# Kernel tuning notes

Hardware: AMD Instinct MI355X
Metric: run time of the kernel (lower is better)

The kernel has to match this reference:

```python
import jax, jax.numpy as jnp
import numpy as np

D = 512      # embeddings_dim (in_features == out_features)
H = 4        # num_heads
MID = 2048   # mid_features
B, S = 4, 2048
EPS = 1e-5


def _ln(x, g, b):
    mu = jnp.mean(x, axis=-1, keepdims=True)
    var = jnp.mean(jnp.square(x - mu), axis=-1, keepdims=True)
    return g * (x - mu) / jnp.sqrt(var + EPS) + b


def setup_inputs() -> dict:
    key = jax.random.key(0)
    ks = jax.random.split(key, 16)
    w = 0.02  # weight init scale
    return {
        "x_encoder": jax.random.normal(ks[0], (B, S, D), jnp.float32),
        "x_decoder": jax.random.normal(ks[1], (B, S, D), jnp.float32),
        # per-head full-width projections (each head is a D->D Linear)
        "Wq": jax.random.normal(ks[2], (H, D, D), jnp.float32) * w,
        "bq": jnp.zeros((H, D), jnp.float32),
        "Wk": jax.random.normal(ks[3], (H, D, D), jnp.float32) * w,
        "bk": jnp.zeros((H, D), jnp.float32),
        "Wv": jax.random.normal(ks[4], (H, D, D), jnp.float32) * w,
        "bv": jnp.zeros((H, D), jnp.float32),
        # out_reshaper: Rearrange('b h s d -> b s (d h)') then Linear(D*H -> D)
        "Wo": jax.random.normal(ks[5], (D * H, D), jnp.float32) * w,
        "bo": jnp.zeros((D,), jnp.float32),
        "ln1_g": jnp.ones((D,), jnp.float32), "ln1_b": jnp.zeros((D,), jnp.float32),
        "ln2_g": jnp.ones((D,), jnp.float32), "ln2_b": jnp.zeros((D,), jnp.float32),
        # FouriFeedForward: D -> MID -> D with SELU
        "W1": jax.random.normal(ks[6], (D, MID), jnp.float32) * w,
        "b1": jnp.zeros((MID,), jnp.float32),
        "W2": jax.random.normal(ks[7], (MID, D), jnp.float32) * w,
        "b2": jnp.zeros((D,), jnp.float32),
        "ln3_g": jnp.ones((D,), jnp.float32), "ln3_b": jnp.zeros((D,), jnp.float32),
    }


def reference(x_encoder, x_decoder, Wq, bq, Wk, bk, Wv, bv, Wo, bo,
              ln1_g, ln1_b, ln2_g, ln2_b, W1, b1, W2, b2, ln3_g, ln3_b):
    # Fourier token mixing: per-batch fftn over (seq, feature) dims, keep real part
    xf = jnp.fft.fftn(x_decoder, axes=(1, 2)).real
    xd = _ln(x_decoder + xf, ln1_g, ln1_b)  # [B,S,D]

    # Linear multi-head attention: q from decoder, k/v from encoder.
    # qs/ks/vs: [B,H,S,D]; softmax over the HEAD axis (dim=1 in torch)
    qs = jax.nn.softmax(jnp.einsum('bsd,hde->bhse', xd, Wq) + bq[None, :, None, :], axis=1)
    ks = jax.nn.softmax(jnp.einsum('bsd,hde->bhse', x_encoder, Wk) + bk[None, :, None, :], axis=1)
    vs = jnp.einsum('bsd,hde->bhse', x_encoder, Wv) + bv[None, :, None, :]

    gc = jnp.einsum('bhsd,bhse->bhde', ks, vs)       # [B,H,D,D] global contexts
    out = jnp.einsum('bhsd,bhde->bhse', qs, gc)      # [B,H,S,D]

    # Rearrange 'b h s d -> b s (d h)': d is the slow axis, h the fast axis
    b, h, s, d = out.shape
    out = out.transpose(0, 2, 3, 1).reshape(b, s, d * h)
    attn = out @ Wo + bo                              # [B,S,D]

    x = _ln(xd + attn, ln2_g, ln2_b)
    ff = jax.nn.selu(x @ W1 + b1) @ W2 + b2           # dropout_p=0 (eval)
    x = _ln(x + ff, ln3_g, ln3_b)
    return x
```

## Files before the change

kernel.cpp:

```cpp
#include <hip/hip_runtime.h>
#include <stdint.h>

typedef __bf16 bf16;
typedef __bf16 bf16x8 __attribute__((ext_vector_type(8)));
typedef float f32x4 __attribute__((ext_vector_type(4)));

static __device__ __forceinline__ void async16(const void* g, void* l) {
  __builtin_amdgcn_global_load_lds(
      (__attribute__((address_space(1))) void*)g,
      (__attribute__((address_space(3))) void*)l, 16, 0, 0);
}

__global__ void __launch_bounds__(256) prep_all(
    const float* __restrict__ xdec, const float* __restrict__ xenc,
    bf16* __restrict__ Ttrig, bf16* __restrict__ Atrig2,
    bf16* __restrict__ xdec_b, bf16* __restrict__ xenc_b,
    const float* __restrict__ Wq, const float* __restrict__ Wk,
    const float* __restrict__ Wv, const float* __restrict__ Wo,
    const float* __restrict__ W1, const float* __restrict__ W2,
    bf16* __restrict__ BtQ, bf16* __restrict__ BtK, bf16* __restrict__ BtV,
    bf16* __restrict__ WoTh, bf16* __restrict__ W1T, bf16* __restrict__ W2T) {
  __shared__ bf16 tile[32][33];
  int id = blockIdx.x;
  if (id < 2048) {
    int idx = id * 256 + threadIdx.x;
    int d = idx & 511, jp = idx >> 9;
    int jj = jp >> 1, p = jp & 1;
    int t = (d * jj) & 511;
    float ang = (float)t * (6.283185307179586f / 512.0f);
    Ttrig[idx] = (bf16)(p ? __sinf(ang) : __cosf(ang));
  } else if (id < 11840) {
    int idx = (id - 2048) * 256 + threadIdx.x;
    int k = idx % 1088;
    int rr = idx / 1088;
    int r = rr % 1152, half = rr / 1152;
    float v = 0.0f;
    int tt = (r * k) & 2047;
    float ang = (float)tt * (6.283185307179586f / 2048.0f);
    if (half == 0) { if (r <= 1024 && k <= 1024) v = __cosf(ang); }
    else           { if (r <= 1023 && k >= 1 && k <= 1023) v = -__sinf(ang); }
    Atrig2[idx] = (bf16)v;
  } else if (id < 15936) {
    int i = ((id - 11840) * 256 + threadIdx.x) * 4;
    float4 v = *(const float4*)(xdec + i);
    bf16 o[4] __attribute__((aligned(8))) =
        {(bf16)v.x, (bf16)v.y, (bf16)v.z, (bf16)v.w};
    *(uint2*)(xdec_b + i) = *(const uint2*)o;
  } else if (id < 20032) {
    int i = ((id - 15936) * 256 + threadIdx.x) * 4;
    float4 v = *(const float4*)(xenc + i);
    bf16 o[4] __attribute__((aligned(8))) =
        {(bf16)v.x, (bf16)v.y, (bf16)v.z, (bf16)v.w};
    *(uint2*)(xenc_b + i) = *(const uint2*)o;
  } else {
    int id2 = id - 20032;
    int kind = id2 >> 10, t = id2 & 1023;
    const float* in; bf16* out; int R, C, rt, ct;
    bool iperm = false, hsel = false; int hh = 0;
    if (kind == 0)      { in = Wq; out = BtQ; R = 2048; C = 512; rt = t >> 4; ct = t & 15; iperm = true; }
    else if (kind == 1) { in = Wk; out = BtK; R = 2048; C = 512; rt = t >> 4; ct = t & 15; iperm = true; }
    else if (kind == 2) { in = Wv; out = BtV; R = 2048; C = 512; rt = t >> 4; ct = t & 15; iperm = true; }
    else if (kind == 3) {
      int zz = t >> 8, tt = t & 255;
      in = Wo; out = WoTh + (long)zz * 262144;
      R = 512; C = 512; rt = tt >> 4; ct = tt & 15; hsel = true; hh = zz;
    }
    else if (kind == 4) { in = W1; out = W1T; R = 512; C = 2048; rt = t >> 6; ct = t & 63; }
    else                { in = W2; out = W2T; R = 2048; C = 512; rt = t >> 4; ct = t & 15; }
    int c0 = ct * 32, r0 = rt * 32;
    int tx = threadIdx.x & 31, ty = threadIdx.x >> 5;
#pragma unroll
    for (int i = 0; i < 32; i += 8) {
      int r = r0 + ty + i;
      int rr = hsel ? (4 * r + hh) : r;
      tile[ty + i][tx] = (bf16)in[(long)rr * C + (c0 + tx)];
    }
    __syncthreads();
#pragma unroll
    for (int i = 0; i < 32; i += 8) {
      int cc = c0 + ty + i, rr = r0 + tx;
      if (iperm) {
        int e = cc, h = rr >> 9;
        int n = (e & 15) | (h << 4) | ((e >> 4) << 6);
        out[((long)n << 9) + (rr & 511)] = tile[tx][ty + i];
      } else {
        out[(long)cc * R + rr] = tile[tx][ty + i];
      }
    }
  }
}

__global__ void __launch_bounds__(256) fold_y(const bf16* __restrict__ Yt,
                                              bf16* __restrict__ Yf2) {
  int idx2 = blockIdx.x * 256 + threadIdx.x;
  int k2 = (idx2 % 544) * 2;
  int rr = idx2 / 544;
  int j = rr & 511, z = rr >> 9;
  int b = z & 3, half = z >> 2;
  const bf16* yin = Yt + (long)b * 2097152 + (long)j * 4096;
  bf16 o[2] __attribute__((aligned(4)));
  if (half == 0) {
    bf16 f[2] __attribute__((aligned(4)));
    *(uint*)f = *(const uint*)(yin + k2);
    float r0 = (float)yin[2048 - k2];
    float r1 = (float)yin[2047 - k2];
    float v0, v1;
    if (k2 == 0)            v0 = (float)f[0];
    else if (k2 == 1024)    v0 = (float)f[0];
    else if (k2 < 1024)     v0 = (float)f[0] + r0;
    else                    v0 = 0.0f;
    if (k2 + 1 < 1024)      v1 = (float)f[1] + r1;
    else                    v1 = 0.0f;
    o[0] = (bf16)v0; o[1] = (bf16)v1;
  } else {
    bf16 f[2] __attribute__((aligned(4)));
    *(uint*)f = *(const uint*)(yin + 2048 + k2);
    float r0 = (float)yin[4096 - k2];
    float r1 = (float)yin[4095 - k2];
    float v0, v1;
    if (k2 >= 1 && k2 <= 1023) v0 = (float)f[0] - r0; else v0 = 0.0f;
    if (k2 + 1 <= 1023)        v1 = (float)f[1] - r1; else v1 = 0.0f;
    o[0] = (bf16)v0; o[1] = (bf16)v1;
  }
  *(uint*)(Yf2 + (long)z * 557056 + (long)j * 1088 + k2) = *(const uint*)o;
}

__global__ void __launch_bounds__(256) ln1_kernel(
    const float* __restrict__ xdec, const bf16* __restrict__ CSb,
    const float* __restrict__ g, const float* __restrict__ be,
    bf16* __restrict__ outb) {
  const int row = blockIdx.x, t = threadIdx.x;
  const int b = row >> 11, s = row & 2047;
  const int sp = (s <= 1024) ? s : 2048 - s;
  const float sgn = (s <= 1024) ? 1.0f : -1.0f;
  const bf16* Crow = CSb + ((long)b * 1152 + sp) * 512;
  const bf16* Srow = CSb + ((long)(b + 4) * 1152 + sp) * 512;
  const long base = (long)row * 512;
  float2 xp = *(const float2*)(xdec + base + 2 * t);
  bf16 cp[2] __attribute__((aligned(4)));
  bf16 spv[2] __attribute__((aligned(4)));
  *(uint*)cp = *(const uint*)(Crow + 2 * t);
  *(uint*)spv = *(const uint*)(Srow + 2 * t);
  float v0 = xp.x + (float)cp[0] + sgn * (float)spv[0];
  float v1 = xp.y + (float)cp[1] + sgn * (float)spv[1];
  float sm = v0 + v1, q = v0 * v0 + v1 * v1;
#pragma unroll
  for (int off = 32; off > 0; off >>= 1) {
    sm += __shfl_down(sm, off);
    q += __shfl_down(q, off);
  }
  __shared__ float red[8];
  const int wv = t >> 6, ln = t & 63;
  if (ln == 0) { red[wv] = sm; red[wv + 4] = q; }
  __syncthreads();
  float S = red[0] + red[1] + red[2] + red[3];
  float Q = red[4] + red[5] + red[6] + red[7];
  float mu = S * (1.0f / 512.0f);
  float var = Q * (1.0f / 512.0f) - mu * mu;
  float rstd = rsqrtf(var + 1e-5f);
  float2 gp = *(const float2*)(g + 2 * t);
  float2 bp = *(const float2*)(be + 2 * t);
  bf16 op[2] __attribute__((aligned(4)));
  op[0] = (bf16)(gp.x * (v0 - mu) * rstd + bp.x);
  op[1] = (bf16)(gp.y * (v1 - mu) * rstd + bp.y);
  *(uint*)(outb + base + 2 * t) = *(const uint*)op;
}

template <int WRITE_BF16, int WRITE_F32>
__global__ void __launch_bounds__(256) ln_kernel(
    const bf16* __restrict__ A, const bf16* __restrict__ Bv,
    const float* __restrict__ g, const float* __restrict__ be,
    bf16* __restrict__ outb, float* __restrict__ outf) {
  const int row = blockIdx.x, t = threadIdx.x;
  const long base = (long)row * 512;
  bf16 ap[2] __attribute__((aligned(4)));
  bf16 bpv[2] __attribute__((aligned(4)));
  *(uint*)ap = *(const uint*)(A + base + 2 * t);
  *(uint*)bpv = *(const uint*)(Bv + base + 2 * t);
  float v0 = (float)ap[0] + (float)bpv[0];
  float v1 = (float)ap[1] + (float)bpv[1];
  float s = v0 + v1, q = v0 * v0 + v1 * v1;
#pragma unroll
  for (int off = 32; off > 0; off >>= 1) {
    s += __shfl_down(s, off);
    q += __shfl_down(q, off);
  }
  __shared__ float red[8];
  const int wv = t >> 6, ln = t & 63;
  if (ln == 0) { red[wv] = s; red[wv + 4] = q; }
  __syncthreads();
  float S = red[0] + red[1] + red[2] + red[3];
  float Q = red[4] + red[5] + red[6] + red[7];
  float mu = S * (1.0f / 512.0f);
  float var = Q * (1.0f / 512.0f) - mu * mu;
  float rstd = rsqrtf(var + 1e-5f);
  float2 gp = *(const float2*)(g + 2 * t);
  float2 bp = *(const float2*)(be + 2 * t);
  float o0 = gp.x * (v0 - mu) * rstd + bp.x;
  float o1 = gp.y * (v1 - mu) * rstd + bp.y;
  if (WRITE_BF16) {
    bf16 op[2] __attribute__((aligned(4)));
    op[0] = (bf16)o0; op[1] = (bf16)o1;
    *(uint*)(outb + base + 2 * t) = *(const uint*)op;
  }
  if (WRITE_F32) {
    float2 of; of.x = o0; of.y = o1;
    *(float2*)(outf + base + 2 * t) = of;
  }
}

template <int BN, int ADDR_MODE, int HAS_BIAS, int DO_SELU, int F32OUT, int SWIZ,
          int AHEAD>
static __device__ __forceinline__ void gemm_bt_body(
    int id, bf16* lA, bf16* lB,
    const bf16* __restrict__ A, const bf16* __restrict__ Bt,
    const float* __restrict__ bias, void* __restrict__ Cout,
    int N, int K, long sAz, long sBz, long sBiasz, long sCz,
    int gx, int gy, int gin) {
  int x, y, z;
  {
    if (SWIZ == 0) {
      x = id % gx; int t2 = id / gx; y = t2 % gy; z = t2 / gy;
    } else {
      int xcd = id & 7, r = id >> 3;
      int inner = r % gin, G = xcd + 8 * (r / gin);
      if (SWIZ == 1)      { y = G; x = inner % gx; z = inner / gx; }
      else if (SWIZ == 2) { z = G; x = inner % gx; y = inner / gx; }
      else                { x = G; y = inner % gy; z = inner / gy; }
    }
  }
  A  += (AHEAD == 1) ? sAz * (z & 3) : (AHEAD == 2) ? sAz * (z >> 2) : sAz * z;
  Bt += sBz * z;
  const int m0 = y * 128, n0 = x * BN;
  const int t = threadIdx.x;
  const int lane = t & 63, wave = t >> 6;
  const int srow = t >> 3;
  const int pch  = t & 7;
  const int lch  = pch ^ (srow & 7);
  const bf16* Ag = A  + (long)(m0 + srow) * K + lch * 8;
  const bf16* Bg = Bt + (long)(n0 + srow) * K + lch * 8;
  bf16* lAp = lA + srow * 64 + pch * 8;
  bf16* lBp = lB + srow * 64 + pch * 8;
  constexpr int MI = (BN == 128) ? 4 : 2;
  const int wm = (BN == 128) ? (wave >> 1) * 64 : wave * 32;
  const int wn = (BN == 128) ? (wave & 1) * 64 : 0;
  const int fr = lane & 15, fq = lane >> 4;

  f32x4 acc[MI][4] = {};

  for (int k0 = 0; k0 < K; k0 += 64) {
    __syncthreads();
#pragma unroll
    for (int i = 0; i < 4; ++i)
      async16(Ag + k0 + (long)(32 * i) * K, lAp + 32 * i * 64);
#pragma unroll
    for (int i = 0; i < BN / 32; ++i)
      async16(Bg + k0 + (long)(32 * i) * K, lBp + 32 * i * 64);
    __syncthreads();
#pragma unroll
    for (int kk = 0; kk < 2; ++kk) {
      bf16x8 av[MI], bfrag[4];
#pragma unroll
      for (int mi = 0; mi < MI; ++mi) {
        int r = wm + mi * 16 + fr;
        int c = (kk * 4 + fq) ^ (r & 7);
        av[mi] = *(const bf16x8*)&lA[r * 64 + c * 8];
      }
#pragma unroll
      for (int ni = 0; ni < 4; ++ni) {
        int r = wn + ni * 16 + fr;
        int c = (kk * 4 + fq) ^ (r & 7);
        bfrag[ni] = *(const bf16x8*)&lB[r * 64 + c * 8];
      }
#pragma unroll
      for (int mi = 0; mi < MI; ++mi)
#pragma unroll
        for (int ni = 0; ni < 4; ++ni)
          acc[mi][ni] = __builtin_amdgcn_mfma_f32_16x16x32_bf16(
              av[mi], bfrag[ni], acc[mi][ni], 0, 0, 0);
    }
  }

#pragma unroll
  for (int mi = 0; mi < MI; ++mi) {
#pragma unroll
    for (int ni = 0; ni < 4; ++ni) {
      const int col = n0 + wn + ni * 16 + fr;
      float bias_v = 0.0f;
      if (HAS_BIAS == 1) bias_v = bias[sBiasz * z + col];
      if (ADDR_MODE == 9) {
        const int b = z >> 2, h = z & 3;
        const int kidx = (col & 15) | (h << 4) | ((col >> 4) << 6);
#pragma unroll
        for (int r = 0; r < 4; ++r) {
          const int row = m0 + wm + mi * 16 + fq * 4 + r;
          ((bf16*)Cout)[((long)(b * 512 + row)) * 2048 + kidx] =
              (bf16)(acc[mi][ni][r] + bias_v);
        }
      } else {
#pragma unroll
        for (int r = 0; r < 4; ++r) {
          const int row = m0 + wm + mi * 16 + fq * 4 + r;
          float v = acc[mi][ni][r] + bias_v;
          if (DO_SELU) v = v > 0.0f ? 1.0507009873554805f * v
                                    : 1.7580993408473766f * (__expf(v) - 1.0f);
          long addr = sCz * z + (long)row * N + col;
          if (F32OUT) ((float*)Cout)[addr] = v;
          else        ((bf16*)Cout)[addr] = (bf16)v;
        }
      }
    }
  }
}

template <int BN, int ADDR_MODE, int HAS_BIAS, int DO_SELU, int F32OUT, int SWIZ,
          int AHEAD = 0>
__global__ void __launch_bounds__(256, 2) gemm_bt(
    const bf16* __restrict__ A, const bf16* __restrict__ Bt,
    const float* __restrict__ bias, void* __restrict__ Cout,
    int N, int K, long sAz, long sBz, long sBiasz, long sCz,
    int gx, int gy, int gin) {
  __shared__ __align__(16) bf16 lA[128 * 64];
  __shared__ __align__(16) bf16 lB[BN * 64];
  gemm_bt_body<BN, ADDR_MODE, HAS_BIAS, DO_SELU, F32OUT, SWIZ, AHEAD>(
      blockIdx.x, lA, lB, A, Bt, bias, Cout, N, K, sAz, sBz, sBiasz, sCz, gx, gy, gin);
}

static __device__ __forceinline__ void qkv_body(
    int id, bf16* lA, bf16* lB,
    const bf16* __restrict__ Aq, const bf16* __restrict__ Aenc,
    const bf16* __restrict__ BQ, const bf16* __restrict__ BK,
    const bf16* __restrict__ BV,
    const float* __restrict__ bq, const float* __restrict__ bk,
    const float* __restrict__ bv,
    bf16* __restrict__ qs2, bf16* __restrict__ ksT, bf16* __restrict__ vsT) {
  const int seg = id >> 10, sid = id & 1023;
  const int xcd = sid & 7, r = sid >> 3;
  const int x = r & 15, y = xcd + 8 * (r >> 4);
  const bf16 *A, *Bt; bf16* out; const float* bias;
  if (seg == 0)      { A = Aq;   Bt = BQ; out = qs2; bias = bq; }
  else if (seg == 1) { A = Aenc; Bt = BK; out = ksT; bias = bk; }
  else               { A = Aenc; Bt = BV; out = vsT; bias = bv; }
  const int K = 512;
  const int m0 = y * 128, n0 = x * 128;
  const int t = threadIdx.x;
  const int lane = t & 63, wave = t >> 6;
  const int srow = t >> 3, pch = t & 7, lch = pch ^ (srow & 7);
  const bf16* Ag = A  + (long)(m0 + srow) * K + lch * 8;
  const bf16* Bg = Bt + (long)(n0 + srow) * K + lch * 8;
  bf16* lAp = lA + srow * 64 + pch * 8;
  bf16* lBp = lB + srow * 64 + pch * 8;
  const int wm = (wave >> 1) * 64, wn = (wave & 1) * 64;
  const int fr = lane & 15, fq = lane >> 4;

  f32x4 acc[4][4] = {};
  for (int k0 = 0; k0 < K; k0 += 64) {
    __syncthreads();
#pragma unroll
    for (int i = 0; i < 4; ++i) {
      async16(Ag + k0 + (long)(32 * i) * K, lAp + 32 * i * 64);
      async16(Bg + k0 + (long)(32 * i) * K, lBp + 32 * i * 64);
    }
    __syncthreads();
#pragma unroll
    for (int kk = 0; kk < 2; ++kk) {
      bf16x8 av[4], bfrag[4];
#pragma unroll
      for (int mi = 0; mi < 4; ++mi) {
        int rr = wm + mi * 16 + fr;
        int c = (kk * 4 + fq) ^ (rr & 7);
        av[mi] = *(const bf16x8*)&lA[rr * 64 + c * 8];
      }
#pragma unroll
      for (int ni = 0; ni < 4; ++ni) {
        int rr = wn + ni * 16 + fr;
        int c = (kk * 4 + fq) ^ (rr & 7);
        bfrag[ni] = *(const bf16x8*)&lB[rr * 64 + c * 8];
      }
#pragma unroll
      for (int mi = 0; mi < 4; ++mi)
#pragma unroll
        for (int ni = 0; ni < 4; ++ni)
          acc[mi][ni] = __builtin_amdgcn_mfma_f32_16x16x32_bf16(
              av[mi], bfrag[ni], acc[mi][ni], 0, 0, 0);
    }
  }

  const int ebase = fr + 16 * ((n0 + wn) >> 6);
  const float b0 = bias[ebase], b1 = bias[512 + ebase],
              b2 = bias[1024 + ebase], b3 = bias[1536 + ebase];
  if (seg == 0) {
#pragma unroll
    for (int mi = 0; mi < 4; ++mi) {
#pragma unroll
      for (int r = 0; r < 4; ++r) {
        const int row = m0 + wm + mi * 16 + fq * 4 + r;
        float v0 = acc[mi][0][r] + b0;
        float v1 = acc[mi][1][r] + b1;
        float v2 = acc[mi][2][r] + b2;
        float v3 = acc[mi][3][r] + b3;
        float m = fmaxf(fmaxf(v0, v1), fmaxf(v2, v3));
        float p0 = __expf(v0 - m), p1 = __expf(v1 - m),
              p2 = __expf(v2 - m), p3 = __expf(v3 - m);
        float rs = 1.0f / (p0 + p1 + p2 + p3);
        const long ob = (long)row * 2048 + n0 + wn + fr;
        out[ob]      = (bf16)(p0 * rs);
        out[ob + 16] = (bf16)(p1 * rs);
        out[ob + 32] = (bf16)(p2 * rs);
        out[ob + 48] = (bf16)(p3 * rs);
      }
    }
  } else {
    bf16* lT = lA;
    const int bb = m0 >> 11;
    const int s_tile = m0 & 2047;
    const int e_loc = fr + 16 * (wn >> 6);
    __syncthreads();
#pragma unroll
    for (int mi = 0; mi < 4; ++mi) {
      const int s0 = wm + mi * 16 + fq * 4;
      bf16 tmp[4][4] __attribute__((aligned(8)));
#pragma unroll
      for (int r = 0; r < 4; ++r) {
        float v0 = acc[mi][0][r] + b0;
        float v1 = acc[mi][1][r] + b1;
        float v2 = acc[mi][2][r] + b2;
        float v3 = acc[mi][3][r] + b3;
        if (seg == 1) {
          float m = fmaxf(fmaxf(v0, v1), fmaxf(v2, v3));
          float p0 = __expf(v0 - m), p1 = __expf(v1 - m),
                p2 = __expf(v2 - m), p3 = __expf(v3 - m);
          float rs = 1.0f / (p0 + p1 + p2 + p3);
          v0 = p0 * rs; v1 = p1 * rs; v2 = p2 * rs; v3 = p3 * rs;
        }
        tmp[0][r] = (bf16)v0; tmp[1][r] = (bf16)v1;
        tmp[2][r] = (bf16)v2; tmp[3][r] = (bf16)v3;
      }
#pragma unroll
      for (int ni = 0; ni < 4; ++ni) {
        const int row = ni * 32 + e_loc;
        const int el = row * 128 + ((((s0 >> 3) ^ (row & 15)) << 3) | (s0 & 7));
        *(uint2*)&lT[el] = *(const uint2*)tmp[ni];
      }
    }
    __syncthreads();
    const int c = lane & 15, rg = lane >> 4;
#pragma unroll
    for (int i = 0; i < 8; ++i) {
      const int row = wave * 32 + rg + i * 4;
      const int el = row * 128 + ((c ^ (row & 15)) << 3);
      uint4 v = *(const uint4*)&lT[el];
      const int h = row >> 5, e = (row & 31) + 32 * x;
      *(uint4*)(out + ((long)((bb * 4 + h) * 512 + e)) * 2048 + s_tile + c * 8) = v;
    }
  }
}

__global__ void __launch_bounds__(256, 2) fused_kv_yt(
    const bf16* __restrict__ Aenc, const bf16* __restrict__ BK,
    const bf16* __restrict__ BV,
    const float* __restrict__ bk, const float* __restrict__ bv,
    bf16* __restrict__ ksT, bf16* __restrict__ vsT,
    const bf16* __restrict__ Ttrig, const bf16* __restrict__ xdec_b,
    bf16* __restrict__ Yt) {
  __shared__ __align__(16) bf16 smem[16384];
  int id = blockIdx.x;
  if (id < 2048)
    qkv_body(id + 1024, smem, smem + 8192, nullptr, Aenc, nullptr, BK, BV,
             nullptr, bk, bv, nullptr, ksT, vsT);
  else
    gemm_bt_body<128, 0, 0, 0, 0, 3, 0>(id - 2048, smem, smem + 8192,
        Ttrig, xdec_b, nullptr, Yt, 2048, 512, 0L, 1048576L, 0L, 2097152L, 16, 8, 32);
}

__global__ void __launch_bounds__(256, 2) fused_gc_cs(
    const bf16* __restrict__ ksT, const bf16* __restrict__ vsT,
    bf16* __restrict__ gc,
    const bf16* __restrict__ Atrig2, const bf16* __restrict__ Yf2,
    bf16* __restrict__ CSb) {
  __shared__ __align__(16) bf16 smem[12288];
  int id = blockIdx.x;
  if (id < 512)
    gemm_bt_body<64, 0, 0, 0, 0, 2, 0>(id, smem, smem + 8192,
        ksT, vsT, nullptr, gc, 512, 2048, 1048576L, 1048576L, 0L, 262144L, 8, 4, 32);
  else
    gemm_bt_body<64, 0, 0, 0, 0, 2, 2>(id - 512, smem, smem + 8192,
        Atrig2, Yf2, nullptr, CSb, 512, 1088, 1253376L, 557056L, 0L, 589824L, 8, 9, 72);
}

__global__ void __launch_bounds__(256, 2) fused_q_gw(
    const bf16* __restrict__ Aq, const bf16* __restrict__ BQ,
    const float* __restrict__ bq, bf16* __restrict__ qs2,
    const bf16* __restrict__ WoTh, const bf16* __restrict__ gc,
    bf16* __restrict__ gwT) {
  __shared__ __align__(16) bf16 smem[16384];
  int id = blockIdx.x;
  if (id < 1024)
    qkv_body(id, smem, smem + 8192, Aq, nullptr, BQ, nullptr, nullptr,
             bq, nullptr, nullptr, qs2, nullptr, nullptr);
  else
    gemm_bt_body<64, 9, 0, 0, 0, 2, 1>(id - 1024, smem, smem + 8192,
        WoTh, gc, nullptr, gwT, 512, 512, 262144L, 262144L, 0L, 0L, 8, 4, 32);
}

extern "C" void kernel_launch(void* const* d_in, const int* in_sizes, int n_in,
                              void* d_out, int out_size, void* d_ws, size_t ws_size,
                              hipStream_t stream) {
  (void)in_sizes; (void)n_in; (void)out_size; (void)ws_size;
  const float* x_enc = (const float*)d_in[0];
  const float* x_dec = (const float*)d_in[1];
  const float* Wq = (const float*)d_in[2];
  const float* bq = (const float*)d_in[3];
  const float* Wk = (const float*)d_in[4];
  const float* bk = (const float*)d_in[5];
  const float* Wv = (const float*)d_in[6];
  const float* bv = (const float*)d_in[7];
  const float* Wo = (const float*)d_in[8];
  const float* bo = (const float*)d_in[9];
  const float* g1 = (const float*)d_in[10];
  const float* be1 = (const float*)d_in[11];
  const float* g2 = (const float*)d_in[12];
  const float* be2 = (const float*)d_in[13];
  const float* W1 = (const float*)d_in[14];
  const float* b1 = (const float*)d_in[15];
  const float* W2 = (const float*)d_in[16];
  const float* b2 = (const float*)d_in[17];
  const float* g3 = (const float*)d_in[18];
  const float* be3 = (const float*)d_in[19];

  char* ws = (char*)d_ws;
  const size_t MB = 1u << 20;
  bf16*  BtQ    = (bf16*) (ws + 0);
  bf16*  midb   = (bf16*) (ws + 0);
  bf16*  ksT    = (bf16*) (ws + 32 * MB);
  bf16*  attn_b = (bf16*) (ws + 32 * MB);
  bf16*  vsT    = (bf16*) (ws + 64 * MB);
  bf16*  ff_b   = (bf16*) (ws + 72 * MB);
  bf16*  Atrig2 = (bf16*) (ws + 96 * MB);
  bf16*  Ttrig  = (bf16*) (ws + 101 * MB);
  bf16*  CSb    = (bf16*) (ws + 102 * MB);
  bf16*  qs2    = (bf16*) (ws + 96 * MB);
  bf16*  xenc_b = (bf16*) (ws + 128 * MB);
  bf16*  BtK    = (bf16*) (ws + 136 * MB);
  bf16*  BtV    = (bf16*) (ws + 138 * MB);
  bf16*  xd_b   = (bf16*) (ws + 192 * MB);
  bf16*  x2_b   = (bf16*) (ws + 200 * MB);
  bf16*  gwT    = (bf16*) (ws + 208 * MB);
  bf16*  Yt     = (bf16*) (ws + 216 * MB);
  bf16*  gc     = (bf16*) (ws + 216 * MB);
  bf16*  Yf2    = (bf16*) (ws + 232 * MB);
  bf16*  WoTh   = (bf16*) (ws + 241 * MB);
  bf16*  W1T    = (bf16*) (ws + 243 * MB);
  bf16*  W2T    = (bf16*) (ws + 245 * MB);
  bf16*  xdec_b = (bf16*) (ws + 247 * MB);

  prep_all<<<26176, 256, 0, stream>>>(x_dec, x_enc, Ttrig, Atrig2, xdec_b, xenc_b,
                                      Wq, Wk, Wv, Wo, W1, W2,
                                      BtQ, BtK, BtV, WoTh, W1T, W2T);

  fused_kv_yt<<<2560, 256, 0, stream>>>(xenc_b, BtK, BtV, bk, bv, ksT, vsT,
                                        Ttrig, xdec_b, Yt);

  fold_y<<<8704, 256, 0, stream>>>(Yt, Yf2);

  fused_gc_cs<<<1088, 256, 0, stream>>>(ksT, vsT, gc, Atrig2, Yf2, CSb);

  ln1_kernel<<<8192, 256, 0, stream>>>(x_dec, CSb, g1, be1, xd_b);

  fused_q_gw<<<1536, 256, 0, stream>>>(xd_b, BtQ, bq, qs2, WoTh, gc, gwT);

  gemm_bt<64, 0, 1, 0, 0, 1><<<512, 256, 0, stream>>>(
      qs2, gwT, bo, attn_b, 512, 2048, 4194304L, 1048576L, 0L, 1048576L, 8, 16, 32);
  ln_kernel<1, 0><<<8192, 256, 0, stream>>>(
      xd_b, attn_b, g2, be2, x2_b, nullptr);

  gemm_bt<128, 0, 1, 1, 0, 1><<<1024, 256, 0, stream>>>(
      x2_b, W1T, b1, midb, 2048, 512, 0L, 0L, 0L, 0L, 16, 64, 16);
  gemm_bt<64, 0, 1, 0, 0, 1><<<512, 256, 0, stream>>>(
      midb, W2T, b2, ff_b, 512, 2048, 0L, 0L, 0L, 0L, 8, 64, 8);
  ln_kernel<0, 1><<<8192, 256, 0, stream>>>(
      x2_b, ff_b, g3, be3, nullptr, (float*)d_out);
}
```

Measured before the change: 366.6 us.

## Fuse K and V projections sharing encoder tile; vectorize trig and fold kernels

New measurement: 355.6 us. 3.0% less time.

```diff
diff --git a/kernel.cpp b/kernel.cpp
--- a/kernel.cpp
+++ b/kernel.cpp
@@ -22,38 +22,49 @@
     bf16* __restrict__ WoTh, bf16* __restrict__ W1T, bf16* __restrict__ W2T) {
   __shared__ bf16 tile[32][33];
   int id = blockIdx.x;
-  if (id < 2048) {
+  if (id < 512) {
     int idx = id * 256 + threadIdx.x;
-    int d = idx & 511, jp = idx >> 9;
+    int d0 = (idx & 127) * 4, jp = idx >> 7;
     int jj = jp >> 1, p = jp & 1;
-    int t = (d * jj) & 511;
-    float ang = (float)t * (6.283185307179586f / 512.0f);
-    Ttrig[idx] = (bf16)(p ? __sinf(ang) : __cosf(ang));
-  } else if (id < 11840) {
-    int idx = (id - 2048) * 256 + threadIdx.x;
-    int k = idx % 1088;
-    int rr = idx / 1088;
+    bf16 o[4] __attribute__((aligned(8)));
+#pragma unroll
+    for (int i = 0; i < 4; ++i) {
+      int tt = ((d0 + i) * jj) & 511;
+      float ang = (float)tt * (6.283185307179586f / 512.0f);
+      o[i] = (bf16)(p ? __sinf(ang) : __cosf(ang));
+    }
+    *(uint2*)(Ttrig + jp * 512 + d0) = *(const uint2*)o;
+  } else if (id < 2960) {
+    int idx = (id - 512) * 256 + threadIdx.x;
+    int k0 = (idx % 272) * 4;
+    int rr = idx / 272;
     int r = rr % 1152, half = rr / 1152;
-    float v = 0.0f;
-    int tt = (r * k) & 2047;
-    float ang = (float)tt * (6.283185307179586f / 2048.0f);
-    if (half == 0) { if (r <= 1024 && k <= 1024) v = __cosf(ang); }
-    else           { if (r <= 1023 && k >= 1 && k <= 1023) v = -__sinf(ang); }
-    Atrig2[idx] = (bf16)v;
-  } else if (id < 15936) {
-    int i = ((id - 11840) * 256 + threadIdx.x) * 4;
+    bf16 o[4] __attribute__((aligned(8)));
+#pragma unroll
+    for (int i = 0; i < 4; ++i) {
+      int k = k0 + i;
+      float v = 0.0f;
+      int tt = (r * k) & 2047;
+      float ang = (float)tt * (6.283185307179586f / 2048.0f);
+      if (half == 0) { if (r <= 1024 && k <= 1024) v = __cosf(ang); }
+      else           { if (r <= 1023 && k >= 1 && k <= 1023) v = -__sinf(ang); }
+      o[i] = (bf16)v;
+    }
+    *(uint2*)(Atrig2 + (long)rr * 1088 + k0) = *(const uint2*)o;
+  } else if (id < 7056) {
+    int i = ((id - 2960) * 256 + threadIdx.x) * 4;
     float4 v = *(const float4*)(xdec + i);
     bf16 o[4] __attribute__((aligned(8))) =
         {(bf16)v.x, (bf16)v.y, (bf16)v.z, (bf16)v.w};
     *(uint2*)(xdec_b + i) = *(const uint2*)o;
-  } else if (id < 20032) {
-    int i = ((id - 15936) * 256 + threadIdx.x) * 4;
+  } else if (id < 11152) {
+    int i = ((id - 7056) * 256 + threadIdx.x) * 4;
     float4 v = *(const float4*)(xenc + i);
     bf16 o[4] __attribute__((aligned(8))) =
         {(bf16)v.x, (bf16)v.y, (bf16)v.z, (bf16)v.w};
     *(uint2*)(xenc_b + i) = *(const uint2*)o;
   } else {
-    int id2 = id - 20032;
+    int id2 = id - 11152;
     int kind = id2 >> 10, t = id2 & 1023;
     const float* in; bf16* out; int R, C, rt, ct;
     bool iperm = false, hsel = false; int hh = 0;
@@ -92,37 +103,38 @@
 
 __global__ void __launch_bounds__(256) fold_y(const bf16* __restrict__ Yt,
                                               bf16* __restrict__ Yf2) {
-  int idx2 = blockIdx.x * 256 + threadIdx.x;
-  int k2 = (idx2 % 544) * 2;
-  int rr = idx2 / 544;
+  int idx = blockIdx.x * 256 + threadIdx.x;
+  int k0 = (idx % 272) * 4;
+  int rr = idx / 272;
   int j = rr & 511, z = rr >> 9;
   int b = z & 3, half = z >> 2;
   const bf16* yin = Yt + (long)b * 2097152 + (long)j * 4096;
-  bf16 o[2] __attribute__((aligned(4)));
+  bf16 o[4] __attribute__((aligned(8)));
   if (half == 0) {
-    bf16 f[2] __attribute__((aligned(4)));
-    *(uint*)f = *(const uint*)(yin + k2);
-    float r0 = (float)yin[2048 - k2];
-    float r1 = (float)yin[2047 - k2];
-    float v0, v1;
-    if (k2 == 0)            v0 = (float)f[0];
-    else if (k2 == 1024)    v0 = (float)f[0];
-    else if (k2 < 1024)     v0 = (float)f[0] + r0;
-    else                    v0 = 0.0f;
-    if (k2 + 1 < 1024)      v1 = (float)f[1] + r1;
-    else                    v1 = 0.0f;
-    o[0] = (bf16)v0; o[1] = (bf16)v1;
+    bf16 f[4] __attribute__((aligned(8)));
+    *(uint2*)f = *(const uint2*)(yin + k0);
+#pragma unroll
+    for (int i = 0; i < 4; ++i) {
+      int k = k0 + i;
+      float v;
+      if (k == 0)            v = (float)f[0];
+      else if (k == 1024)    v = (float)f[i];
+      else if (k < 1024)     v = (float)f[i] + (float)yin[2048 - k];
+      else                   v = 0.0f;
+      o[i] = (bf16)v;
+    }
   } else {
-    bf16 f[2] __attribute__((aligned(4)));
-    *(uint*)f = *(const uint*)(yin + 2048 + k2);
-    float r0 = (float)yin[4096 - k2];
-    float r1 = (float)yin[4095 - k2];
-    float v0, v1;
-    if (k2 >= 1 && k2 <= 1023) v0 = (float)f[0] - r0; else v0 = 0.0f;
-    if (k2 + 1 <= 1023)        v1 = (float)f[1] - r1; else v1 = 0.0f;
-    o[0] = (bf16)v0; o[1] = (bf16)v1;
-  }
-  *(uint*)(Yf2 + (long)z * 557056 + (long)j * 1088 + k2) = *(const uint*)o;
+    bf16 f[4] __attribute__((aligned(8)));
+    *(uint2*)f = *(const uint2*)(yin + 2048 + k0);
+#pragma unroll
+    for (int i = 0; i < 4; ++i) {
+      int k = k0 + i;
+      float v = 0.0f;
+      if (k >= 1 && k <= 1023) v = (float)f[i] - (float)yin[4096 - k];
+      o[i] = (bf16)v;
+    }
+  }
+  *(uint2*)(Yf2 + (long)z * 557056 + (long)j * 1088 + k0) = *(const uint2*)o;
 }
 
 __global__ void __launch_bounds__(256) ln1_kernel(
@@ -334,13 +346,11 @@
     const float* __restrict__ bq, const float* __restrict__ bk,
     const float* __restrict__ bv,
     bf16* __restrict__ qs2, bf16* __restrict__ ksT, bf16* __restrict__ vsT) {
-  const int seg = id >> 10, sid = id & 1023;
+  const int sid = id & 1023;
   const int xcd = sid & 7, r = sid >> 3;
   const int x = r & 15, y = xcd + 8 * (r >> 4);
-  const bf16 *A, *Bt; bf16* out; const float* bias;
-  if (seg == 0)      { A = Aq;   Bt = BQ; out = qs2; bias = bq; }
-  else if (seg == 1) { A = Aenc; Bt = BK; out = ksT; bias = bk; }
-  else               { A = Aenc; Bt = BV; out = vsT; bias = bv; }
+  const bf16 *A = Aq, *Bt = BQ; bf16* out = qs2; const float* bias = bq;
+  (void)Aenc; (void)BK; (void)BV; (void)bk; (void)bv; (void)ksT; (void)vsT;
   const int K = 512;
   const int m0 = y * 128, n0 = x * 128;
   const int t = threadIdx.x;
@@ -389,70 +399,164 @@
   const int ebase = fr + 16 * ((n0 + wn) >> 6);
   const float b0 = bias[ebase], b1 = bias[512 + ebase],
               b2 = bias[1024 + ebase], b3 = bias[1536 + ebase];
-  if (seg == 0) {
-#pragma unroll
-    for (int mi = 0; mi < 4; ++mi) {
-#pragma unroll
-      for (int r = 0; r < 4; ++r) {
-        const int row = m0 + wm + mi * 16 + fq * 4 + r;
-        float v0 = acc[mi][0][r] + b0;
-        float v1 = acc[mi][1][r] + b1;
-        float v2 = acc[mi][2][r] + b2;
-        float v3 = acc[mi][3][r] + b3;
-        float m = fmaxf(fmaxf(v0, v1), fmaxf(v2, v3));
-        float p0 = __expf(v0 - m), p1 = __expf(v1 - m),
-              p2 = __expf(v2 - m), p3 = __expf(v3 - m);
-        float rs = 1.0f / (p0 + p1 + p2 + p3);
-        const long ob = (long)row * 2048 + n0 + wn + fr;
-        out[ob]      = (bf16)(p0 * rs);
-        out[ob + 16] = (bf16)(p1 * rs);
-        out[ob + 32] = (bf16)(p2 * rs);
-        out[ob + 48] = (bf16)(p3 * rs);
-      }
-    }
-  } else {
-    bf16* lT = lA;
-    const int bb = m0 >> 11;
-    const int s_tile = m0 & 2047;
-    const int e_loc = fr + 16 * (wn >> 6);
+#pragma unroll
+  for (int mi = 0; mi < 4; ++mi) {
+#pragma unroll
+    for (int r = 0; r < 4; ++r) {
+      const int row = m0 + wm + mi * 16 + fq * 4 + r;
+      float v0 = acc[mi][0][r] + b0;
+      float v1 = acc[mi][1][r] + b1;
+      float v2 = acc[mi][2][r] + b2;
+      float v3 = acc[mi][3][r] + b3;
+      float m = fmaxf(fmaxf(v0, v1), fmaxf(v2, v3));
+      float p0 = __expf(v0 - m), p1 = __expf(v1 - m),
+            p2 = __expf(v2 - m), p3 = __expf(v3 - m);
+      float rs = 1.0f / (p0 + p1 + p2 + p3);
+      const long ob = (long)row * 2048 + n0 + wn + fr;
+      out[ob]      = (bf16)(p0 * rs);
+      out[ob + 16] = (bf16)(p1 * rs);
+      out[ob + 32] = (bf16)(p2 * rs);
+      out[ob + 48] = (bf16)(p3 * rs);
+    }
+  }
+}
+
+static __device__ __forceinline__ void kv2_body(
+    int sid, bf16* smem,
+    const bf16* __restrict__ Aenc, const bf16* __restrict__ BK,
+    const bf16* __restrict__ BV,
+    const float* __restrict__ bk, const float* __restrict__ bv,
+    bf16* __restrict__ ksT, bf16* __restrict__ vsT) {
+  const int xcd = sid & 7, r = sid >> 3;
+  const int x = r & 15, y = xcd + 8 * (r >> 4);
+  const int K = 512;
+  const int m0 = y * 128, n0 = x * 128;
+  const int t = threadIdx.x;
+  const int lane = t & 63, wave = t >> 6;
+  const int srow = t >> 3, pch = t & 7, lch = pch ^ (srow & 7);
+  bf16* lA  = smem;
+  bf16* lBK = smem + 8192;
+  bf16* lBV = smem + 16384;
+  const bf16* Ag  = Aenc + (long)(m0 + srow) * K + lch * 8;
+  const bf16* BKg = BK   + (long)(n0 + srow) * K + lch * 8;
+  const bf16* BVg = BV   + (long)(n0 + srow) * K + lch * 8;
+  bf16* lAp  = lA  + srow * 64 + pch * 8;
+  bf16* lBKp = lBK + srow * 64 + pch * 8;
+  bf16* lBVp = lBV + srow * 64 + pch * 8;
+  const int wm = (wave >> 1) * 64, wn = (wave & 1) * 64;
+  const int fr = lane & 15, fq = lane >> 4;
+
+  f32x4 accK[4][4] = {}, accV[4][4] = {};
+  for (int k0 = 0; k0 < K; k0 += 64) {
     __syncthreads();
 #pragma unroll
-    for (int mi = 0; mi < 4; ++mi) {
-      const int s0 = wm + mi * 16 + fq * 4;
-      bf16 tmp[4][4] __attribute__((aligned(8)));
-#pragma unroll
-      for (int r = 0; r < 4; ++r) {
-        float v0 = acc[mi][0][r] + b0;
-        float v1 = acc[mi][1][r] + b1;
-        float v2 = acc[mi][2][r] + b2;
-        float v3 = acc[mi][3][r] + b3;
-        if (seg == 1) {
-          float m = fmaxf(fmaxf(v0, v1), fmaxf(v2, v3));
-          float p0 = __expf(v0 - m), p1 = __expf(v1 - m),
-                p2 = __expf(v2 - m), p3 = __expf(v3 - m);
-          float rs = 1.0f / (p0 + p1 + p2 + p3);
-          v0 = p0 * rs; v1 = p1 * rs; v2 = p2 * rs; v3 = p3 * rs;
+    for (int i = 0; i < 4; ++i) {
+      async16(Ag  + k0 + (long)(32 * i) * K, lAp  + 32 * i * 64);
+      async16(BKg + k0 + (long)(32 * i) * K, lBKp + 32 * i * 64);
+      async16(BVg + k0 + (long)(32 * i) * K, lBVp + 32 * i * 64);
+    }
+    __syncthreads();
+#pragma unroll
+    for (int kk = 0; kk < 2; ++kk) {
+      bf16x8 av[4], bkf[4], bvf[4];
+#pragma unroll
+      for (int mi = 0; mi < 4; ++mi) {
+        int rr = wm + mi * 16 + fr;
+        int c = (kk * 4 + fq) ^ (rr & 7);
+        av[mi] = *(const bf16x8*)&lA[rr * 64 + c * 8];
+      }
+#pragma unroll
+      for (int ni = 0; ni < 4; ++ni) {
+        int rr = wn + ni * 16 + fr;
+        int c = (kk * 4 + fq) ^ (rr & 7);
+        bkf[ni] = *(const bf16x8*)&lBK[rr * 64 + c * 8];
+        bvf[ni] = *(const bf16x8*)&lBV[rr * 64 + c * 8];
+      }
+#pragma unroll
+      for (int mi = 0; mi < 4; ++mi)
+#pragma unroll
+        for (int ni = 0; ni < 4; ++ni) {
+          accK[mi][ni] = __builtin_amdgcn_mfma_f32_16x16x32_bf16(
+              av[mi], bkf[ni], accK[mi][ni], 0, 0, 0);
+          accV[mi][ni] = __builtin_amdgcn_mfma_f32_16x16x32_bf16(
+              av[mi], bvf[ni], accV[mi][ni], 0, 0, 0);
         }
-        tmp[0][r] = (bf16)v0; tmp[1][r] = (bf16)v1;
-        tmp[2][r] = (bf16)v2; tmp[3][r] = (bf16)v3;
-      }
-#pragma unroll
-      for (int ni = 0; ni < 4; ++ni) {
-        const int row = ni * 32 + e_loc;
-        const int el = row * 128 + ((((s0 >> 3) ^ (row & 15)) << 3) | (s0 & 7));
-        *(uint2*)&lT[el] = *(const uint2*)tmp[ni];
-      }
-    }
-    __syncthreads();
-    const int c = lane & 15, rg = lane >> 4;
-#pragma unroll
-    for (int i = 0; i < 8; ++i) {
-      const int row = wave * 32 + rg + i * 4;
-      const int el = row * 128 + ((c ^ (row & 15)) << 3);
-      uint4 v = *(const uint4*)&lT[el];
-      const int h = row >> 5, e = (row & 31) + 32 * x;
-      *(uint4*)(out + ((long)((bb * 4 + h) * 512 + e)) * 2048 + s_tile + c * 8) = v;
-    }
+    }
+  }
+
+  const int ebase = fr + 16 * ((n0 + wn) >> 6);
+  const float kb0 = bk[ebase], kb1 = bk[512 + ebase],
+              kb2 = bk[1024 + ebase], kb3 = bk[1536 + ebase];
+  const float vb0 = bv[ebase], vb1 = bv[512 + ebase],
+              vb2 = bv[1024 + ebase], vb3 = bv[1536 + ebase];
+  bf16* lT = smem;
+  const int bb = m0 >> 11;
+  const int s_tile = m0 & 2047;
+  const int e_loc = fr + 16 * (wn >> 6);
+  const int c = lane & 15, rg = lane >> 4;
+
+  __syncthreads();
+#pragma unroll
+  for (int mi = 0; mi < 4; ++mi) {
+    const int s0 = wm + mi * 16 + fq * 4;
+    bf16 tmp[4][4] __attribute__((aligned(8)));
+#pragma unroll
+    for (int r2 = 0; r2 < 4; ++r2) {
+      float v0 = accK[mi][0][r2] + kb0;
+      float v1 = accK[mi][1][r2] + kb1;
+      float v2 = accK[mi][2][r2] + kb2;
+      float v3 = accK[mi][3][r2] + kb3;
+      float m = fmaxf(fmaxf(v0, v1), fmaxf(v2, v3));
+      float p0 = __expf(v0 - m), p1 = __expf(v1 - m),
+            p2 = __expf(v2 - m), p3 = __expf(v3 - m);
+      float rs = 1.0f / (p0 + p1 + p2 + p3);
+      tmp[0][r2] = (bf16)(p0 * rs); tmp[1][r2] = (bf16)(p1 * rs);
+      tmp[2][r2] = (bf16)(p2 * rs); tmp[3][r2] = (bf16)(p3 * rs);
+    }
+#pragma unroll
+    for (int ni = 0; ni < 4; ++ni) {
+      const int row = ni * 32 + e_loc;
+      const int el = row * 128 + ((((s0 >> 3) ^ (row & 15)) << 3) | (s0 & 7));
+      *(uint2*)&lT[el] = *(const uint2*)tmp[ni];
+    }
+  }
+  __syncthreads();
+#pragma unroll
+  for (int i = 0; i < 8; ++i) {
+    const int row = wave * 32 + rg + i * 4;
+    const int el = row * 128 + ((c ^ (row & 15)) << 3);
+    uint4 v = *(const uint4*)&lT[el];
+    const int h = row >> 5, e = (row & 31) + 32 * x;
+    *(uint4*)(ksT + ((long)((bb * 4 + h) * 512 + e)) * 2048 + s_tile + c * 8) = v;
+  }
+
+  __syncthreads();
+#pragma unroll
+  for (int mi = 0; mi < 4; ++mi) {
+    const int s0 = wm + mi * 16 + fq * 4;
+    bf16 tmp[4][4] __attribute__((aligned(8)));
+#pragma unroll
+    for (int r2 = 0; r2 < 4; ++r2) {
+      tmp[0][r2] = (bf16)(accV[mi][0][r2] + vb0);
+      tmp[1][r2] = (bf16)(accV[mi][1][r2] + vb1);
+      tmp[2][r2] = (bf16)(accV[mi][2][r2] + vb2);
+      tmp[3][r2] = (bf16)(accV[mi][3][r2] + vb3);
+    }
+#pragma unroll
+    for (int ni = 0; ni < 4; ++ni) {
+      const int row = ni * 32 + e_loc;
+      const int el = row * 128 + ((((s0 >> 3) ^ (row & 15)) << 3) | (s0 & 7));
+      *(uint2*)&lT[el] = *(const uint2*)tmp[ni];
+    }
+  }
+  __syncthreads();
+#pragma unroll
+  for (int i = 0; i < 8; ++i) {
+    const int row = wave * 32 + rg + i * 4;
+    const int el = row * 128 + ((c ^ (row & 15)) << 3);
+    uint4 v = *(const uint4*)&lT[el];
+    const int h = row >> 5, e = (row & 31) + 32 * x;
+    *(uint4*)(vsT + ((long)((bb * 4 + h) * 512 + e)) * 2048 + s_tile + c * 8) = v;
   }
 }
 
@@ -463,13 +567,12 @@
     bf16* __restrict__ ksT, bf16* __restrict__ vsT,
     const bf16* __restrict__ Ttrig, const bf16* __restrict__ xdec_b,
     bf16* __restrict__ Yt) {
-  __shared__ __align__(16) bf16 smem[16384];
+  __shared__ __align__(16) bf16 smem[24576];
   int id = blockIdx.x;
-  if (id < 2048)
-    qkv_body(id + 1024, smem, smem + 8192, nullptr, Aenc, nullptr, BK, BV,
-             nullptr, bk, bv, nullptr, ksT, vsT);
+  if (id < 1024)
+    kv2_body(id, smem, Aenc, BK, BV, bk, bv, ksT, vsT);
   else
-    gemm_bt_body<128, 0, 0, 0, 0, 3, 0>(id - 2048, smem, smem + 8192,
+    gemm_bt_body<128, 0, 0, 0, 0, 3, 0>(id - 1024, smem, smem + 8192,
         Ttrig, xdec_b, nullptr, Yt, 2048, 512, 0L, 1048576L, 0L, 2097152L, 16, 8, 32);
 }
 
@@ -554,14 +657,14 @@
   bf16*  W2T    = (bf16*) (ws + 245 * MB);
   bf16*  xdec_b = (bf16*) (ws + 247 * MB);
 
-  prep_all<<<26176, 256, 0, stream>>>(x_dec, x_enc, Ttrig, Atrig2, xdec_b, xenc_b,
+  prep_all<<<17296, 256, 0, stream>>>(x_dec, x_enc, Ttrig, Atrig2, xdec_b, xenc_b,
                                       Wq, Wk, Wv, Wo, W1, W2,
                                       BtQ, BtK, BtV, WoTh, W1T, W2T);
 
-  fused_kv_yt<<<2560, 256, 0, stream>>>(xenc_b, BtK, BtV, bk, bv, ksT, vsT,
+  fused_kv_yt<<<1536, 256, 0, stream>>>(xenc_b, BtK, BtV, bk, bv, ksT, vsT,
                                         Ttrig, xdec_b, Yt);
 
-  fold_y<<<8704, 256, 0, stream>>>(Yt, Yf2);
+  fold_y<<<4352, 256, 0, stream>>>(Yt, Yf2);
 
   fused_gc_cs<<<1088, 256, 0, stream>>>(ksT, vsT, gc, Atrig2, Yf2, CSb);
 
```
